# Optimization experiments

Hardware: AMD Instinct MI355X
Metric: run time of the kernel (lower is better)

Reference implementation:

```python
import jax, jax.numpy as jnp
import numpy as np

B, T, C, H = 4, 2048, 1024, 16


def setup_inputs() -> dict:
    key = jax.random.key(0)
    ks = jax.random.split(key, 5)
    s_attn = 1.0 / np.sqrt(C)
    s_proj = 1.0 / np.sqrt(C)
    return {
        "x": jax.random.normal(ks[0], (B, T, C), dtype=jnp.float32),
        "w_attn": jax.random.uniform(ks[1], (3 * C, C), dtype=jnp.float32, minval=-s_attn, maxval=s_attn),
        "b_attn": jax.random.uniform(ks[2], (3 * C,), dtype=jnp.float32, minval=-s_attn, maxval=s_attn),
        "w_proj": jax.random.uniform(ks[3], (C, C), dtype=jnp.float32, minval=-s_proj, maxval=s_proj),
        "b_proj": jax.random.uniform(ks[4], (C,), dtype=jnp.float32, minval=-s_proj, maxval=s_proj),
    }


def reference(x, w_attn, b_attn, w_proj, b_proj):
    b, t, c = x.shape
    hd = c // H  # head dim
    qkv = jnp.einsum('btc,dc->btd', x, w_attn) + b_attn  # [B,T,3C]
    q, k, v = jnp.split(qkv, 3, axis=-1)
    # [B,H,T,hd]
    q = q.reshape(b, t, H, hd).transpose(0, 2, 1, 3)
    k = k.reshape(b, t, H, hd).transpose(0, 2, 1, 3)
    v = v.reshape(b, t, H, hd).transpose(0, 2, 1, 3)
    att = jnp.einsum('bhqd,bhkd->bhqk', q, k) * (1.0 / np.sqrt(hd))
    mask = jnp.tril(jnp.ones((t, t), dtype=bool))  # causal
    att = jnp.where(mask, att, -jnp.inf)
    att = jax.nn.softmax(att, axis=-1)
    y = jnp.einsum('bhqk,bhkd->bhqd', att, v)
    y = y.transpose(0, 2, 1, 3).reshape(b, t, c)
    return jnp.einsum('btc,dc->btd', y, w_proj) + b_proj
```

## Files before the change

kernel.cpp:

```cpp
#include <hip/hip_runtime.h>

#define Bb 4
#define Tt 2048
#define Cc 1024
#define Hh 16
#define NQKV 3072
#define Mtot 8192

typedef __bf16 bf16_t;
typedef unsigned short u16;
typedef __bf16 bf16x8 __attribute__((ext_vector_type(8)));
typedef __bf16 bf16x4 __attribute__((ext_vector_type(4)));
typedef short short4v __attribute__((ext_vector_type(4)));
typedef float f32x4 __attribute__((ext_vector_type(4)));
typedef float f32x16 __attribute__((ext_vector_type(16)));
typedef unsigned uint2v __attribute__((ext_vector_type(2)));

union bfu { bf16_t b; u16 u; };
union trpair { short4v h[2]; bf16x8 v; };
union pfu { unsigned u[4]; bf16x8 v; };

#define QSCALE 0.18033688011112042f

#define TRD(dst, addr, OFF)                                                     \
  asm volatile("ds_read_b64_tr_b16 %0, %1 offset:" OFF                          \
               : "=v"(dst) : "v"(addr) : "memory")

__device__ __forceinline__ unsigned cvtpk(float a, float b) {
  unsigned r;
  asm("v_cvt_pk_bf16_f32 %0, %1, %2" : "=v"(r) : "v"(a), "v"(b));
  return r;
}
__device__ __forceinline__ uint2v plswap(unsigned a, unsigned b) {
  return __builtin_amdgcn_permlane32_swap(a, b, false, false);
}

__device__ __forceinline__ void cvt8(const float* s, u16* d, size_t i, float f) {
  float4 a = *(const float4*)(s + i);
  float4 b = *(const float4*)(s + i + 4);
  bf16x8 v;
  v[0]=(bf16_t)(a.x*f); v[1]=(bf16_t)(a.y*f); v[2]=(bf16_t)(a.z*f); v[3]=(bf16_t)(a.w*f);
  v[4]=(bf16_t)(b.x*f); v[5]=(bf16_t)(b.y*f); v[6]=(bf16_t)(b.z*f); v[7]=(bf16_t)(b.w*f);
  *(bf16x8*)(d + i) = v;
}

__global__ __launch_bounds__(256) void cvt_all(
    const float* __restrict__ x, const float* __restrict__ w_attn,
    const float* __restrict__ w_proj, const float* __restrict__ b_attn,
    u16* __restrict__ xb, u16* __restrict__ wab, u16* __restrict__ wpb,
    float* __restrict__ sbias)
{
  const int blk = blockIdx.x;
  if (blk < 4096) {
    size_t i = ((size_t)blk * 256 + threadIdx.x) * 8;
    cvt8(x, xb, i, 1.0f);
  } else if (blk < 5632) {
    size_t i = ((size_t)(blk - 4096) * 256 + threadIdx.x) * 8;
    cvt8(w_attn, wab, i, (i < (size_t)Cc * Cc) ? QSCALE : 1.0f);
  } else if (blk < 6144) {
    size_t i = ((size_t)(blk - 5632) * 256 + threadIdx.x) * 8;
    cvt8(w_proj, wpb, i, 1.0f);
  } else {
    int i0 = (blk - 6144) * 2048 + threadIdx.x * 8;
#pragma unroll
    for (int j = 0; j < 8; ++j) {
      int i = i0 + j;
      if (i < NQKV) sbias[i] = b_attn[i] * ((i < Cc) ? QSCALE : 1.0f);
    }
  }
}

template <int OUTBF16>
__global__ __launch_bounds__(256) void gemm_bf16(
    const u16* __restrict__ A, const u16* __restrict__ Bm,
    const float* __restrict__ bias, void* __restrict__ Cout,
    int M, int N, int K)
{
  __shared__ __attribute__((aligned(16))) u16 sa[128][40];
  __shared__ __attribute__((aligned(16))) u16 sb[128][40];

  const int tid  = threadIdx.x;
  const int lane = tid & 63;
  const int wid  = tid >> 6;
  const int wr   = (wid >> 1) * 64;
  const int wc   = (wid & 1) * 64;
  const int l15  = lane & 15;
  const int lh   = lane >> 4;
  const int bm   = blockIdx.x * 128;
  const int bn   = blockIdx.y * 128;

  f32x4 acc[4][4] = {};

  const int srow = tid >> 1;
  const int sseg = (tid & 1) * 16;

  const u16* pa = A  + (size_t)(bm + srow) * K + sseg;
  const u16* pb = Bm + (size_t)(bn + srow) * K + sseg;

  uint4 ar0 = *(const uint4*)pa, ar1 = *(const uint4*)(pa + 8);
  uint4 br0 = *(const uint4*)pb, br1 = *(const uint4*)(pb + 8);
  pa += 32; pb += 32;

  for (int k0 = 0; k0 < K; k0 += 32) {
    __syncthreads();
    *(uint4*)&sa[srow][sseg]     = ar0;
    *(uint4*)&sa[srow][sseg + 8] = ar1;
    *(uint4*)&sb[srow][sseg]     = br0;
    *(uint4*)&sb[srow][sseg + 8] = br1;
    __syncthreads();
    if (k0 + 32 < K) {
      ar0 = *(const uint4*)pa; ar1 = *(const uint4*)(pa + 8);
      br0 = *(const uint4*)pb; br1 = *(const uint4*)(pb + 8);
      pa += 32; pb += 32;
    }
    bf16x8 af[4], bfv[4];
#pragma unroll
    for (int mi = 0; mi < 4; mi++)
      af[mi] = *(const bf16x8*)&sa[wr + mi*16 + l15][lh * 8];
#pragma unroll
    for (int ni = 0; ni < 4; ni++)
      bfv[ni] = *(const bf16x8*)&sb[wc + ni*16 + l15][lh * 8];
#pragma unroll
    for (int mi = 0; mi < 4; mi++)
#pragma unroll
      for (int ni = 0; ni < 4; ni++)
        acc[mi][ni] = __builtin_amdgcn_mfma_f32_16x16x32_bf16(
            af[mi], bfv[ni], acc[mi][ni], 0, 0, 0);
  }

#pragma unroll
  for (int mi = 0; mi < 4; mi++) {
#pragma unroll
    for (int ni = 0; ni < 4; ni++) {
      const int col = bn + wc + ni*16 + l15;
      const float bs = bias[col];
#pragma unroll
      for (int r = 0; r < 4; r++) {
        const int row = bm + wr + mi*16 + lh*4 + r;
        const float val = acc[mi][ni][r] + bs;
        if (OUTBF16) {
          bfu cv; cv.b = (bf16_t)val;
          ((u16*)Cout)[(size_t)row * N + col] = cv.u;
        } else {
          ((float*)Cout)[(size_t)row * N + col] = val;
        }
      }
    }
  }
}

__global__ __launch_bounds__(512, 4) void attn_kernel(
    const u16* __restrict__ qkv, u16* __restrict__ y)
{
  __shared__ __attribute__((aligned(16))) u16 smem[18432];

  const int tid  = threadIdx.x;
  const int lane = tid & 63;
  const int w    = tid >> 6;
  const int l31  = lane & 31;
  const int hh   = lane >> 5;
  const int l15  = lane & 15;
  const int lh   = lane >> 4;
  const int bh   = blockIdx.y;
  const int b    = bh >> 4;
  const int head = bh & 15;

  const size_t rowbase = (size_t)b * Tt * NQKV;

  const int skey = tid >> 3;
  const int sp   = tid & 7;
  const u16* kbase = qkv + rowbase + 1024 + head*64 + sp*8;
  const u16* vbase = qkv + rowbase + 2048 + head*64 + sp*8;

  const unsigned smemB = (unsigned)(size_t)(&smem[0]);
  const unsigned vaddr = smemB + 9216
      + ((lh>>1)*8 + (l15>>2))*144 + (lh&1)*32 + (l15&3)*8;

  for (int half = 0; half < 2; ++half) {
    const int qx    = half ? (7 - (int)blockIdx.x) : (int)blockIdx.x;
    const int qbase = qx * 256;
    const int qw    = qbase + w * 32;
    const int qi    = qw + l31;
    const int ktiles = 4*qx + 4;

    bf16x8 qfrag[4];
#pragma unroll
    for (int m = 0; m < 4; ++m)
      qfrag[m] = *(const bf16x8*)(qkv + rowbase + (size_t)qi * NQKV
                                  + head*64 + m*16 + hh*8);

    f32x16 o0 = {}, o1 = {};
    float m_run = -1e30f, l_part = 0.0f;

    uint4 kr0 = *(const uint4*)(kbase + (size_t)skey * NQKV);
    uint4 vr0 = *(const uint4*)(vbase + (size_t)skey * NQKV);

    for (int kt = 0; kt < ktiles; ++kt) {
      __syncthreads();
      *(uint4*)&smem[skey*72 + sp*8]        = kr0;
      *(uint4*)&smem[4608 + skey*72 + sp*8] = vr0;
      __syncthreads();

      if (kt + 1 < ktiles) {
        kr0 = *(const uint4*)(kbase + (size_t)((kt+1)*64 + skey) * NQKV);
        vr0 = *(const uint4*)(vbase + (size_t)((kt+1)*64 + skey) * NQKV);
      }

      if (kt*64 <= qw + 31) {
        f32x16 s0 = {}, s1 = {};
#pragma unroll
        for (int m = 0; m < 4; ++m) {
          const int co = m*16 + hh*8;
          bf16x8 k0 = *(const bf16x8*)&smem[(l31)*72      + co];
          bf16x8 k1 = *(const bf16x8*)&smem[(32 + l31)*72 + co];
          s0 = __builtin_amdgcn_mfma_f32_32x32x16_bf16(k0, qfrag[m], s0, 0,0,0);
          s1 = __builtin_amdgcn_mfma_f32_32x32x16_bf16(k1, qfrag[m], s1, 0,0,0);
        }

        if (kt*64 + 63 > qw) {
          const int kb0 = kt*64;
#pragma unroll
          for (int r = 0; r < 16; ++r) {
            const int crow = (r&3) + 8*(r>>2) + 4*hh;
            if (kb0 + crow > qi)      s0[r] = -1e30f;
            if (kb0 + 32 + crow > qi) s1[r] = -1e30f;
          }
        }

        float rm = s0[0];
#pragma unroll
        for (int r = 1; r < 16; ++r) rm = fmaxf(rm, s0[r]);
#pragma unroll
        for (int r = 0; r < 16; ++r) rm = fmaxf(rm, s1[r]);
        {
          uint2v t = plswap(__float_as_uint(rm), __float_as_uint(rm));
          rm = fmaxf(__uint_as_float(t[0]), __uint_as_float(t[1]));
        }
        if (__any(rm > m_run + 8.0f)) {
          const float mn = fmaxf(m_run, rm);
          const float al = exp2f(m_run - mn);
          m_run = mn; l_part *= al;
#pragma unroll
          for (int r = 0; r < 16; ++r) { o0[r] *= al; o1[r] *= al; }
        }

        pfu pf0, pf1, pf2, pf3;
        {
          float pe[16];
#pragma unroll
          for (int r = 0; r < 16; ++r) { pe[r] = exp2f(s0[r] - m_run); l_part += pe[r]; }
          unsigned a0 = cvtpk(pe[0],pe[1]),  a1 = cvtpk(pe[2],pe[3]);
          unsigned a2 = cvtpk(pe[4],pe[5]),  a3 = cvtpk(pe[6],pe[7]);
          uint2v x1 = plswap(a0, a2), x2 = plswap(a1, a3);
          pf0.u[0]=x1[0]; pf0.u[1]=x2[0]; pf0.u[2]=x1[1]; pf0.u[3]=x2[1];
          unsigned b0 = cvtpk(pe[8],pe[9]),  b1 = cvtpk(pe[10],pe[11]);
          unsigned b2 = cvtpk(pe[12],pe[13]), b3 = cvtpk(pe[14],pe[15]);
          uint2v x3 = plswap(b0, b2), x4 = plswap(b1, b3);
          pf1.u[0]=x3[0]; pf1.u[1]=x4[0]; pf1.u[2]=x3[1]; pf1.u[3]=x4[1];
        }
        {
          float pe[16];
#pragma unroll
          for (int r = 0; r < 16; ++r) { pe[r] = exp2f(s1[r] - m_run); l_part += pe[r]; }
          unsigned a0 = cvtpk(pe[0],pe[1]),  a1 = cvtpk(pe[2],pe[3]);
          unsigned a2 = cvtpk(pe[4],pe[5]),  a3 = cvtpk(pe[6],pe[7]);
          uint2v x1 = plswap(a0, a2), x2 = plswap(a1, a3);
          pf2.u[0]=x1[0]; pf2.u[1]=x2[0]; pf2.u[2]=x1[1]; pf2.u[3]=x2[1];
          unsigned b0 = cvtpk(pe[8],pe[9]),  b1 = cvtpk(pe[10],pe[11]);
          unsigned b2 = cvtpk(pe[12],pe[13]), b3 = cvtpk(pe[14],pe[15]);
          uint2v x3 = plswap(b0, b2), x4 = plswap(b1, b3);
          pf3.u[0]=x3[0]; pf3.u[1]=x4[0]; pf3.u[2]=x3[1]; pf3.u[3]=x4[1];
        }

        short4v ta0,tb0,ta1,tb1,ta2,tb2,ta3,tb3,ta4,tb4,ta5,tb5,ta6,tb6,ta7,tb7;
        TRD(ta0, vaddr, "0");    TRD(tb0, vaddr, "576");
        TRD(ta1, vaddr, "64");   TRD(tb1, vaddr, "640");
        TRD(ta2, vaddr, "2304"); TRD(tb2, vaddr, "2880");
        TRD(ta3, vaddr, "2368"); TRD(tb3, vaddr, "2944");
        TRD(ta4, vaddr, "4608"); TRD(tb4, vaddr, "5184");
        TRD(ta5, vaddr, "4672"); TRD(tb5, vaddr, "5248");
        TRD(ta6, vaddr, "6912"); TRD(tb6, vaddr, "7488");
        TRD(ta7, vaddr, "6976"); TRD(tb7, vaddr, "7552");
        asm volatile("s_waitcnt lgkmcnt(0)" ::: "memory");
        __builtin_amdgcn_sched_barrier(0);
        trpair v00,v01,v10,v11,v20,v21,v30,v31;
        v00.h[0]=ta0; v00.h[1]=tb0;  v01.h[0]=ta1; v01.h[1]=tb1;
        v10.h[0]=ta2; v10.h[1]=tb2;  v11.h[0]=ta3; v11.h[1]=tb3;
        v20.h[0]=ta4; v20.h[1]=tb4;  v21.h[0]=ta5; v21.h[1]=tb5;
        v30.h[0]=ta6; v30.h[1]=tb6;  v31.h[0]=ta7; v31.h[1]=tb7;
        o0 = __builtin_amdgcn_mfma_f32_32x32x16_bf16(v00.v, pf0.v, o0, 0,0,0);
        o1 = __builtin_amdgcn_mfma_f32_32x32x16_bf16(v01.v, pf0.v, o1, 0,0,0);
        o0 = __builtin_amdgcn_mfma_f32_32x32x16_bf16(v10.v, pf1.v, o0, 0,0,0);
        o1 = __builtin_amdgcn_mfma_f32_32x32x16_bf16(v11.v, pf1.v, o1, 0,0,0);
        o0 = __builtin_amdgcn_mfma_f32_32x32x16_bf16(v20.v, pf2.v, o0, 0,0,0);
        o1 = __builtin_amdgcn_mfma_f32_32x32x16_bf16(v21.v, pf2.v, o1, 0,0,0);
        o0 = __builtin_amdgcn_mfma_f32_32x32x16_bf16(v30.v, pf3.v, o0, 0,0,0);
        o1 = __builtin_amdgcn_mfma_f32_32x32x16_bf16(v31.v, pf3.v, o1, 0,0,0);
      }
    }

    {
      uint2v t = plswap(__float_as_uint(l_part), __float_as_uint(l_part));
      l_part = __uint_as_float(t[0]) + __uint_as_float(t[1]);
    }
    const float inv = 1.0f / l_part;

    __syncthreads();
#pragma unroll
    for (int k4 = 0; k4 < 4; ++k4) {
      bf16x4 pa, pb;
#pragma unroll
      for (int j = 0; j < 4; ++j) {
        pa[j] = (bf16_t)(o0[4*k4 + j] * inv);
        pb[j] = (bf16_t)(o1[4*k4 + j] * inv);
      }
      *(bf16x4*)&smem[w*2304 + l31*72 +      8*k4 + 4*hh] = pa;
      *(bf16x4*)&smem[w*2304 + l31*72 + 32 + 8*k4 + 4*hh] = pb;
    }
    u16* yp = y + ((size_t)(b*Tt + qi)) * Cc + head*64;
#pragma unroll
    for (int p = 0; p < 4; ++p) {
      bf16x8 row = *(const bf16x8*)&smem[w*2304 + l31*72 + p*16 + hh*8];
      *(bf16x8*)(yp + p*16 + hh*8) = row;
    }
  }
}

extern "C" void kernel_launch(void* const* d_in, const int* in_sizes, int n_in,
                              void* d_out, int out_size, void* d_ws, size_t ws_size,
                              hipStream_t stream) {
  const float* x      = (const float*)d_in[0];
  const float* w_attn = (const float*)d_in[1];
  const float* b_attn = (const float*)d_in[2];
  const float* w_proj = (const float*)d_in[3];
  const float* b_proj = (const float*)d_in[4];
  float* out = (float*)d_out;

  char* ws = (char*)d_ws;
  u16*   xb    = (u16*)(ws + 0);
  u16*   wab   = (u16*)(ws + 16777216);
  u16*   wpb   = (u16*)(ws + 23068672);
  u16*   qkvb  = (u16*)(ws + 25165824);
  u16*   yb    = (u16*)(ws + 75497472);
  float* sbias = (float*)(ws + 92274688);

  cvt_all<<<6146, 256, 0, stream>>>(x, w_attn, w_proj, b_attn,
                                    xb, wab, wpb, sbias);

  gemm_bf16<1><<<dim3(Mtot/128, NQKV/128), 256, 0, stream>>>(
      xb, wab, sbias, (void*)qkvb, Mtot, NQKV, Cc);

  attn_kernel<<<dim3(4, Bb*Hh), 512, 0, stream>>>(qkvb, yb);

  gemm_bf16<0><<<dim3(Mtot/128, Cc/128), 256, 0, stream>>>(
      yb, wpb, b_proj, (void*)out, Mtot, Cc, Cc);
}
```

Before: 184.8 us.

## Software-pipeline attention with triple-buffered K/V tiles and QK lookahead

```diff
diff --git a/kernel.cpp b/kernel.cpp
--- a/kernel.cpp
+++ b/kernel.cpp
@@ -149,10 +149,12 @@
   }
 }
 
-__global__ __launch_bounds__(512, 4) void attn_kernel(
+#define BUFU 9216
+
+__global__ __launch_bounds__(512) void attn_kernel(
     const u16* __restrict__ qkv, u16* __restrict__ y)
 {
-  __shared__ __attribute__((aligned(16))) u16 smem[18432];
+  __shared__ __attribute__((aligned(16))) u16 smem[3 * BUFU];
 
   const int tid  = threadIdx.x;
   const int lane = tid & 63;
@@ -173,8 +175,18 @@
   const u16* vbase = qkv + rowbase + 2048 + head*64 + sp*8;
 
   const unsigned smemB = (unsigned)(size_t)(&smem[0]);
-  const unsigned vaddr = smemB + 9216
+  const unsigned trl = smemB
       + ((lh>>1)*8 + (l15>>2))*144 + (lh&1)*32 + (l15&3)*8;
+
+  uint4 kr0, vr0;
+#define LOADREGS(t) do {                                                        \
+    kr0 = *(const uint4*)(kbase + (size_t)((t)*64 + skey) * NQKV);              \
+    vr0 = *(const uint4*)(vbase + (size_t)((t)*64 + skey) * NQKV);              \
+  } while (0)
+#define STAGEB(bofs) do {                                                       \
+    *(uint4*)&smem[(bofs) + skey*72 + sp*8]        = kr0;                       \
+    *(uint4*)&smem[(bofs) + 4608 + skey*72 + sp*8] = vr0;                       \
+  } while (0)
 
   for (int half = 0; half < 2; ++half) {
     const int qx    = half ? (7 - (int)blockIdx.x) : (int)blockIdx.x;
@@ -191,112 +203,148 @@
 
     f32x16 o0 = {}, o1 = {};
     float m_run = -1e30f, l_part = 0.0f;
-
-    uint4 kr0 = *(const uint4*)(kbase + (size_t)skey * NQKV);
-    uint4 vr0 = *(const uint4*)(vbase + (size_t)skey * NQKV);
-
-    for (int kt = 0; kt < ktiles; ++kt) {
+    f32x16 sA0, sA1, sB0, sB1;
+
+    auto qk = [&](f32x16& t0, f32x16& t1, int kofs, int kb0) {
+      f32x16 a0 = {}, a1 = {};
+      __builtin_amdgcn_s_setprio(1);
+#pragma unroll
+      for (int m = 0; m < 4; ++m) {
+        const int co = m*16 + hh*8;
+        bf16x8 k0 = *(const bf16x8*)&smem[kofs + l31*72 + co];
+        bf16x8 k1 = *(const bf16x8*)&smem[kofs + (32 + l31)*72 + co];
+        a0 = __builtin_amdgcn_mfma_f32_32x32x16_bf16(k0, qfrag[m], a0, 0,0,0);
+        a1 = __builtin_amdgcn_mfma_f32_32x32x16_bf16(k1, qfrag[m], a1, 0,0,0);
+      }
+      __builtin_amdgcn_s_setprio(0);
+      if (kb0 + 63 > qw) {
+#pragma unroll
+        for (int r = 0; r < 16; ++r) {
+          const int crow = (r&3) + 8*(r>>2) + 4*hh;
+          if (kb0 + crow > qi)      a0[r] = -1e30f;
+          if (kb0 + 32 + crow > qi) a1[r] = -1e30f;
+        }
+      }
+      t0 = a0; t1 = a1;
+    };
+
+    auto smpv = [&](f32x16& s0, f32x16& s1, int bofs) {
+      float mx[8];
+#pragma unroll
+      for (int i = 0; i < 8; ++i)
+        mx[i] = fmaxf(fmaxf(s0[i], s0[i+8]), fmaxf(s1[i], s1[i+8]));
+#pragma unroll
+      for (int i = 0; i < 4; ++i) mx[i] = fmaxf(mx[i], mx[i+4]);
+      mx[0] = fmaxf(mx[0], mx[2]); mx[1] = fmaxf(mx[1], mx[3]);
+      float rm = fmaxf(mx[0], mx[1]);
+      {
+        uint2v t = plswap(__float_as_uint(rm), __float_as_uint(rm));
+        rm = fmaxf(__uint_as_float(t[0]), __uint_as_float(t[1]));
+      }
+      if (__any(rm > m_run + 8.0f)) {
+        const float mn = fmaxf(m_run, rm);
+        const float al = exp2f(m_run - mn);
+        m_run = mn; l_part *= al;
+#pragma unroll
+        for (int r = 0; r < 16; ++r) { o0[r] *= al; o1[r] *= al; }
+      }
+
+      pfu pf0, pf1, pf2, pf3;
+      float lp0 = 0.f, lp1 = 0.f, lp2 = 0.f, lp3 = 0.f;
+      {
+        float pe[16];
+#pragma unroll
+        for (int r = 0; r < 16; ++r) pe[r] = exp2f(s0[r] - m_run);
+#pragma unroll
+        for (int r = 0; r < 4; ++r) {
+          lp0 += pe[r]; lp1 += pe[4+r]; lp2 += pe[8+r]; lp3 += pe[12+r];
+        }
+        unsigned a0 = cvtpk(pe[0],pe[1]),  a1 = cvtpk(pe[2],pe[3]);
+        unsigned a2 = cvtpk(pe[4],pe[5]),  a3 = cvtpk(pe[6],pe[7]);
+        uint2v x1 = plswap(a0, a2), x2 = plswap(a1, a3);
+        pf0.u[0]=x1[0]; pf0.u[1]=x2[0]; pf0.u[2]=x1[1]; pf0.u[3]=x2[1];
+        unsigned b0 = cvtpk(pe[8],pe[9]),  b1 = cvtpk(pe[10],pe[11]);
+        unsigned b2 = cvtpk(pe[12],pe[13]), b3 = cvtpk(pe[14],pe[15]);
+        uint2v x3 = plswap(b0, b2), x4 = plswap(b1, b3);
+        pf1.u[0]=x3[0]; pf1.u[1]=x4[0]; pf1.u[2]=x3[1]; pf1.u[3]=x4[1];
+      }
+      {
+        float pe[16];
+#pragma unroll
+        for (int r = 0; r < 16; ++r) pe[r] = exp2f(s1[r] - m_run);
+#pragma unroll
+        for (int r = 0; r < 4; ++r) {
+          lp0 += pe[r]; lp1 += pe[4+r]; lp2 += pe[8+r]; lp3 += pe[12+r];
+        }
+        unsigned a0 = cvtpk(pe[0],pe[1]),  a1 = cvtpk(pe[2],pe[3]);
+        unsigned a2 = cvtpk(pe[4],pe[5]),  a3 = cvtpk(pe[6],pe[7]);
+        uint2v x1 = plswap(a0, a2), x2 = plswap(a1, a3);
+        pf2.u[0]=x1[0]; pf2.u[1]=x2[0]; pf2.u[2]=x1[1]; pf2.u[3]=x2[1];
+        unsigned b0 = cvtpk(pe[8],pe[9]),  b1 = cvtpk(pe[10],pe[11]);
+        unsigned b2 = cvtpk(pe[12],pe[13]), b3 = cvtpk(pe[14],pe[15]);
+        uint2v x3 = plswap(b0, b2), x4 = plswap(b1, b3);
+        pf3.u[0]=x3[0]; pf3.u[1]=x4[0]; pf3.u[2]=x3[1]; pf3.u[3]=x4[1];
+      }
+      l_part += (lp0 + lp1) + (lp2 + lp3);
+
+      const unsigned va = trl + (unsigned)(bofs*2 + 9216);
+      short4v ta0,tb0,ta1,tb1,ta2,tb2,ta3,tb3,ta4,tb4,ta5,tb5,ta6,tb6,ta7,tb7;
+      TRD(ta0, va, "0");    TRD(tb0, va, "576");
+      TRD(ta1, va, "64");   TRD(tb1, va, "640");
+      TRD(ta2, va, "2304"); TRD(tb2, va, "2880");
+      TRD(ta3, va, "2368"); TRD(tb3, va, "2944");
+      TRD(ta4, va, "4608"); TRD(tb4, va, "5184");
+      TRD(ta5, va, "4672"); TRD(tb5, va, "5248");
+      TRD(ta6, va, "6912"); TRD(tb6, va, "7488");
+      TRD(ta7, va, "6976"); TRD(tb7, va, "7552");
+      asm volatile("s_waitcnt lgkmcnt(0)" ::: "memory");
+      __builtin_amdgcn_sched_barrier(0);
+      trpair v00,v01,v10,v11,v20,v21,v30,v31;
+      v00.h[0]=ta0; v00.h[1]=tb0;  v01.h[0]=ta1; v01.h[1]=tb1;
+      v10.h[0]=ta2; v10.h[1]=tb2;  v11.h[0]=ta3; v11.h[1]=tb3;
+      v20.h[0]=ta4; v20.h[1]=tb4;  v21.h[0]=ta5; v21.h[1]=tb5;
+      v30.h[0]=ta6; v30.h[1]=tb6;  v31.h[0]=ta7; v31.h[1]=tb7;
+      __builtin_amdgcn_s_setprio(1);
+      o0 = __builtin_amdgcn_mfma_f32_32x32x16_bf16(v00.v, pf0.v, o0, 0,0,0);
+      o1 = __builtin_amdgcn_mfma_f32_32x32x16_bf16(v01.v, pf0.v, o1, 0,0,0);
+      o0 = __builtin_amdgcn_mfma_f32_32x32x16_bf16(v10.v, pf1.v, o0, 0,0,0);
+      o1 = __builtin_amdgcn_mfma_f32_32x32x16_bf16(v11.v, pf1.v, o1, 0,0,0);
+      o0 = __builtin_amdgcn_mfma_f32_32x32x16_bf16(v20.v, pf2.v, o0, 0,0,0);
+      o1 = __builtin_amdgcn_mfma_f32_32x32x16_bf16(v21.v, pf2.v, o1, 0,0,0);
+      o0 = __builtin_amdgcn_mfma_f32_32x32x16_bf16(v30.v, pf3.v, o0, 0,0,0);
+      o1 = __builtin_amdgcn_mfma_f32_32x32x16_bf16(v31.v, pf3.v, o1, 0,0,0);
+      __builtin_amdgcn_s_setprio(0);
+    };
+
+    LOADREGS(0);
+    __syncthreads();
+    STAGEB(0);
+    LOADREGS(1);
+    __syncthreads();
+    qk(sA0, sA1, 0, 0);
+    STAGEB(BUFU);
+    LOADREGS(2);
+
+    int cofs = 0, nofs = BUFU, fofs = 2*BUFU;
+
+    for (int kt = 0; kt < ktiles; kt += 2) {
       __syncthreads();
-      *(uint4*)&smem[skey*72 + sp*8]        = kr0;
-      *(uint4*)&smem[4608 + skey*72 + sp*8] = vr0;
+      if ((kt+1)*64 <= qw + 31) qk(sB0, sB1, nofs, (kt+1)*64);
+      if (kt*64 <= qw + 31)     smpv(sA0, sA1, cofs);
+      if (kt + 2 < ktiles) {
+        STAGEB(fofs);
+        if (kt + 3 < ktiles) LOADREGS(kt + 3);
+      }
+      { int t = cofs; cofs = nofs; nofs = fofs; fofs = t; }
+
       __syncthreads();
-
-      if (kt + 1 < ktiles) {
-        kr0 = *(const uint4*)(kbase + (size_t)((kt+1)*64 + skey) * NQKV);
-        vr0 = *(const uint4*)(vbase + (size_t)((kt+1)*64 + skey) * NQKV);
-      }
-
-      if (kt*64 <= qw + 31) {
-        f32x16 s0 = {}, s1 = {};
-#pragma unroll
-        for (int m = 0; m < 4; ++m) {
-          const int co = m*16 + hh*8;
-          bf16x8 k0 = *(const bf16x8*)&smem[(l31)*72      + co];
-          bf16x8 k1 = *(const bf16x8*)&smem[(32 + l31)*72 + co];
-          s0 = __builtin_amdgcn_mfma_f32_32x32x16_bf16(k0, qfrag[m], s0, 0,0,0);
-          s1 = __builtin_amdgcn_mfma_f32_32x32x16_bf16(k1, qfrag[m], s1, 0,0,0);
-        }
-
-        if (kt*64 + 63 > qw) {
-          const int kb0 = kt*64;
-#pragma unroll
-          for (int r = 0; r < 16; ++r) {
-            const int crow = (r&3) + 8*(r>>2) + 4*hh;
-            if (kb0 + crow > qi)      s0[r] = -1e30f;
-            if (kb0 + 32 + crow > qi) s1[r] = -1e30f;
-          }
-        }
-
-        float rm = s0[0];
-#pragma unroll
-        for (int r = 1; r < 16; ++r) rm = fmaxf(rm, s0[r]);
-#pragma unroll
-        for (int r = 0; r < 16; ++r) rm = fmaxf(rm, s1[r]);
-        {
-          uint2v t = plswap(__float_as_uint(rm), __float_as_uint(rm));
-          rm = fmaxf(__uint_as_float(t[0]), __uint_as_float(t[1]));
-        }
-        if (__any(rm > m_run + 8.0f)) {
-          const float mn = fmaxf(m_run, rm);
-          const float al = exp2f(m_run - mn);
-          m_run = mn; l_part *= al;
-#pragma unroll
-          for (int r = 0; r < 16; ++r) { o0[r] *= al; o1[r] *= al; }
-        }
-
-        pfu pf0, pf1, pf2, pf3;
-        {
-          float pe[16];
-#pragma unroll
-          for (int r = 0; r < 16; ++r) { pe[r] = exp2f(s0[r] - m_run); l_part += pe[r]; }
-          unsigned a0 = cvtpk(pe[0],pe[1]),  a1 = cvtpk(pe[2],pe[3]);
-          unsigned a2 = cvtpk(pe[4],pe[5]),  a3 = cvtpk(pe[6],pe[7]);
-          uint2v x1 = plswap(a0, a2), x2 = plswap(a1, a3);
-          pf0.u[0]=x1[0]; pf0.u[1]=x2[0]; pf0.u[2]=x1[1]; pf0.u[3]=x2[1];
-          unsigned b0 = cvtpk(pe[8],pe[9]),  b1 = cvtpk(pe[10],pe[11]);
-          unsigned b2 = cvtpk(pe[12],pe[13]), b3 = cvtpk(pe[14],pe[15]);
-          uint2v x3 = plswap(b0, b2), x4 = plswap(b1, b3);
-          pf1.u[0]=x3[0]; pf1.u[1]=x4[0]; pf1.u[2]=x3[1]; pf1.u[3]=x4[1];
-        }
-        {
-          float pe[16];
-#pragma unroll
-          for (int r = 0; r < 16; ++r) { pe[r] = exp2f(s1[r] - m_run); l_part += pe[r]; }
-          unsigned a0 = cvtpk(pe[0],pe[1]),  a1 = cvtpk(pe[2],pe[3]);
-          unsigned a2 = cvtpk(pe[4],pe[5]),  a3 = cvtpk(pe[6],pe[7]);
-          uint2v x1 = plswap(a0, a2), x2 = plswap(a1, a3);
-          pf2.u[0]=x1[0]; pf2.u[1]=x2[0]; pf2.u[2]=x1[1]; pf2.u[3]=x2[1];
-          unsigned b0 = cvtpk(pe[8],pe[9]),  b1 = cvtpk(pe[10],pe[11]);
-          unsigned b2 = cvtpk(pe[12],pe[13]), b3 = cvtpk(pe[14],pe[15]);
-          uint2v x3 = plswap(b0, b2), x4 = plswap(b1, b3);
-          pf3.u[0]=x3[0]; pf3.u[1]=x4[0]; pf3.u[2]=x3[1]; pf3.u[3]=x4[1];
-        }
-
-        short4v ta0,tb0,ta1,tb1,ta2,tb2,ta3,tb3,ta4,tb4,ta5,tb5,ta6,tb6,ta7,tb7;
-        TRD(ta0, vaddr, "0");    TRD(tb0, vaddr, "576");
-        TRD(ta1, vaddr, "64");   TRD(tb1, vaddr, "640");
-        TRD(ta2, vaddr, "2304"); TRD(tb2, vaddr, "2880");
-        TRD(ta3, vaddr, "2368"); TRD(tb3, vaddr, "2944");
-        TRD(ta4, vaddr, "4608"); TRD(tb4, vaddr, "5184");
-        TRD(ta5, vaddr, "4672"); TRD(tb5, vaddr, "5248");
-        TRD(ta6, vaddr, "6912"); TRD(tb6, vaddr, "7488");
-        TRD(ta7, vaddr, "6976"); TRD(tb7, vaddr, "7552");
-        asm volatile("s_waitcnt lgkmcnt(0)" ::: "memory");
-        __builtin_amdgcn_sched_barrier(0);
-        trpair v00,v01,v10,v11,v20,v21,v30,v31;
-        v00.h[0]=ta0; v00.h[1]=tb0;  v01.h[0]=ta1; v01.h[1]=tb1;
-        v10.h[0]=ta2; v10.h[1]=tb2;  v11.h[0]=ta3; v11.h[1]=tb3;
-        v20.h[0]=ta4; v20.h[1]=tb4;  v21.h[0]=ta5; v21.h[1]=tb5;
-        v30.h[0]=ta6; v30.h[1]=tb6;  v31.h[0]=ta7; v31.h[1]=tb7;
-        o0 = __builtin_amdgcn_mfma_f32_32x32x16_bf16(v00.v, pf0.v, o0, 0,0,0);
-        o1 = __builtin_amdgcn_mfma_f32_32x32x16_bf16(v01.v, pf0.v, o1, 0,0,0);
-        o0 = __builtin_amdgcn_mfma_f32_32x32x16_bf16(v10.v, pf1.v, o0, 0,0,0);
-        o1 = __builtin_amdgcn_mfma_f32_32x32x16_bf16(v11.v, pf1.v, o1, 0,0,0);
-        o0 = __builtin_amdgcn_mfma_f32_32x32x16_bf16(v20.v, pf2.v, o0, 0,0,0);
-        o1 = __builtin_amdgcn_mfma_f32_32x32x16_bf16(v21.v, pf2.v, o1, 0,0,0);
-        o0 = __builtin_amdgcn_mfma_f32_32x32x16_bf16(v30.v, pf3.v, o0, 0,0,0);
-        o1 = __builtin_amdgcn_mfma_f32_32x32x16_bf16(v31.v, pf3.v, o1, 0,0,0);
-      }
+      if ((kt+2) < ktiles && (kt+2)*64 <= qw + 31) qk(sA0, sA1, nofs, (kt+2)*64);
+      if ((kt+1)*64 <= qw + 31) smpv(sB0, sB1, cofs);
+      if (kt + 3 < ktiles) {
+        STAGEB(fofs);
+        if (kt + 4 < ktiles) LOADREGS(kt + 4);
+      }
+      { int t = cofs; cofs = nofs; nofs = fofs; fofs = t; }
     }
 
     {
@@ -324,6 +372,8 @@
       *(bf16x8*)(yp + p*16 + hh*8) = row;
     }
   }
+#undef LOADREGS
+#undef STAGEB
 }
 
 extern "C" void kernel_launch(void* const* d_in, const int* in_sizes, int n_in,
```

Measured after the change: 181.8 us, median of 2. No clear change (-1.6%).
